# Kernel tuning notes

Measured on AMD Instinct MI355X. Metric: run time of the kernel, lower is better.

The kernel has to match this reference:

```python
import jax, jax.numpy as jnp
import numpy as np
from jax import lax

B, S, I, H, O = 64, 512, 512, 1024, 2


def setup_inputs() -> dict:
    key = jax.random.key(0)
    ks = jax.random.split(key, 16)
    sc = 0.02
    def w(k, shape):
        return jax.random.normal(k, shape, dtype=jnp.float32) * sc
    inp = {
        "x": jax.random.normal(ks[0], (B, S, I), dtype=jnp.float32),
        # layer 0 GRU gates: Linear(I+H, H)
        "Wr0": w(ks[1], (H, I + H)), "br0": jnp.zeros((H,), jnp.float32),
        "Wz0": w(ks[2], (H, I + H)), "bz0": jnp.zeros((H,), jnp.float32),
        "Wc0": w(ks[3], (H, I + H)), "bc0": jnp.zeros((H,), jnp.float32),
        # layer 1 GRU gates: Linear(H+H, H)
        "Wr1": w(ks[4], (H, 2 * H)), "br1": jnp.zeros((H,), jnp.float32),
        "Wz1": w(ks[5], (H, 2 * H)), "bz1": jnp.zeros((H,), jnp.float32),
        "Wc1": w(ks[6], (H, 2 * H)), "bc1": jnp.zeros((H,), jnp.float32),
        "Wreg": w(ks[7], (O, H)), "breg": jnp.zeros((O,), jnp.float32),
    }
    return inp


def _gru_cell(h, xin, Wr, br, Wz, bz, Wc, bc):
    # Faithful to source GRUCell: note h*z + (1-z)*can (inverted vs standard GRU).
    xh = jnp.concatenate([xin, h], axis=1)
    r = jax.nn.sigmoid(xh @ Wr.T + br)
    z = jax.nn.sigmoid(xh @ Wz.T + bz)
    can = jnp.tanh(jnp.concatenate([xin, h * r], axis=1) @ Wc.T + bc)
    return h * z + (1.0 - z) * can


def reference(x, Wr0, br0, Wz0, bz0, Wc0, bc0, Wr1, br1, Wz1, bz1, Wc1, bc1, Wreg, breg):
    b = x.shape[0]
    hdim = Wr0.shape[0]
    h0_init = jnp.zeros((b, hdim), x.dtype)
    h1_init = jnp.zeros((b, hdim), x.dtype)

    def step(carry, xt):
        h0, h1 = carry
        h0 = _gru_cell(h0, xt, Wr0, br0, Wz0, bz0, Wc0, bc0)
        h1 = _gru_cell(h1, h0, Wr1, br1, Wz1, bz1, Wc1, bc1)
        return (h0, h1), None

    xs = jnp.swapaxes(x, 0, 1)  # [S, B, I]
    (h0, h1), _ = lax.scan(step, (h0_init, h1_init), xs)
    return h1 @ Wreg.T + breg
```

## Files before the change

### kernel.cpp

```cpp
#include <hip/hip_runtime.h>


typedef _Float16 f16;
typedef f16  f16x8 __attribute__((ext_vector_type(8)));
typedef float f32x4 __attribute__((ext_vector_type(4)));
typedef unsigned long long u64;

#define NB   64
#define SEQ  512
#define IDIM 512
#define HDIM 1024
#define NBH  (NB*HDIM)

#define OFF_H0   0u
#define OFF_H1   262144u
#define OFF_H0R  524288u
#define OFF_H1R  655360u
#define OFF_FLA  786432u
#define OFF_FLB  787456u
#define OFF_W16  790528u
#define W16_L0_ELEMS 4718592u

#define SMEM_BYTES 37888

#define MFMA16 __builtin_amdgcn_mfma_f32_16x16x32_f16

__device__ __forceinline__ float sigf(float x){ return 1.0f/(1.0f+__expf(-x)); }
__device__ __forceinline__ float tanh_fast(float x){ float e=__expf(2.0f*x); return 1.0f - 2.0f/(e+1.0f); }

__device__ __forceinline__ f16x8 cload16(const f16* p){
  f16x8 r;
  asm volatile("global_load_dwordx4 %0, %1, off sc0 sc1" : "=v"(r) : "v"(p));
  return r;
}
__device__ __forceinline__ void cstore16(f16* p, f16x8 v){
  asm volatile("global_store_dwordx4 %0, %1, off sc0 sc1" :: "v"(p), "v"(v) : "memory");
}

__device__ __forceinline__ f16x8 load_x_frag(const float* p){
  f32x4 v0 = *(const f32x4*)p;
  f32x4 v1 = *(const f32x4*)(p+4);
  f16x8 r;
  r[0]=(f16)v0[0]; r[1]=(f16)v0[1]; r[2]=(f16)v0[2]; r[3]=(f16)v0[3];
  r[4]=(f16)v1[0]; r[5]=(f16)v1[1]; r[6]=(f16)v1[2]; r[7]=(f16)v1[3];
  return r;
}

template<int LAYER>
__device__ void run_rnn(int g, int n32, const float* x,
    const float* brp, const float* bzp, const float* bcp,
    char* ws, char* smem, unsigned* flA, unsigned* flB, int slotB){
  constexpr int K   = (LAYER==0) ? 1536 : 2048;
  constexpr int NKS = K/32;
  constexpr int KW  = NKS/8;
  constexpr int XKS = (LAYER==0) ? 16 : 32;
  const int tid  = threadIdx.x;
  const int lane = tid & 63;
  const int kg   = tid >> 6;
  const int quad = lane >> 4;
  const int qo   = quad*8;
  const int m_base = g*16;
  const int n_base = n32*32;
  const int arow   = m_base + (lane & 15);

  f32x4* red = (f32x4*)smem;
  float* zst = (float*)(smem + 32768);
  f16*   hst = (f16*)  (smem + 34816);
  float* hf  = (float*)(smem + 35840);

  hf[tid & 511] = 0.f;
  __syncthreads();

  f16* h0m = (f16*)(ws + OFF_H0);
  f16* h1m = (f16*)(ws + OFF_H1);
  f16* hrbuf = (LAYER==0) ? (f16*)(ws + OFF_H0R) : (f16*)(ws + OFF_H1R);
  f16* hown  = (LAYER==0) ? h0m : h1m;
  const char* w16L = ws + OFF_W16 + (LAYER ? (size_t)W16_L0_ELEMS*2 : 0);

  const size_t lo = (size_t)lane*16;
  const int nt0 = n32*2, nt1 = n32*2 + 1;
  const char* bR0 = w16L + ((size_t)((0*64 + nt0)*NKS + kg*KW))*1024 + lo;
  const char* bR1 = w16L + ((size_t)((0*64 + nt1)*NKS + kg*KW))*1024 + lo;
  const char* bZ0 = w16L + ((size_t)((1*64 + nt0)*NKS + kg*KW))*1024 + lo;
  const char* bZ1 = w16L + ((size_t)((1*64 + nt1)*NKS + kg*KW))*1024 + lo;
  const char* bC0 = w16L + ((size_t)((2*64 + nt0)*NKS + kg*KW))*1024 + lo;
  const char* bC1 = w16L + ((size_t)((2*64 + nt1)*NKS + kg*KW))*1024 + lo;

  const int col_own = n_base + (kg & 1)*16 + (lane & 15);
  const float bRv = brp[col_own], bZv = bzp[col_own], bCv = bcp[col_own];

  unsigned lgA = 0, lgB = 0;
  f16x8 fa[KW];
  f16x8 xf[KW];

  if (LAYER==0){
#pragma unroll
    for (int j=0;j<KW;++j){
      int ks = kg*KW + j;
      if (ks < XKS) xf[j] = load_x_frag(x + ((size_t)arow*SEQ + 0)*IDIM + ks*32 + qo);
    }
  }

  for (int iter = 0; iter <= SEQ; ++iter){
    const bool act  = (LAYER==0) ? (iter < SEQ) : (iter >= 1);
    const int  bufA = (iter & 1) ^ 1;

    f32x4 aC0{0,0,0,0}, aC1{0,0,0,0};

    if (act){
#pragma unroll
      for (int j=0;j<KW;++j){
        int ks = kg*KW + j;
        if (LAYER==0){
          if (ks >= XKS)
            fa[j] = cload16(h0m + (size_t)bufA*NBH + (size_t)arow*HDIM + (ks-16)*32 + qo);
        } else {
          if (ks < 32)
            fa[j] = cload16(h0m + (size_t)bufA*NBH + (size_t)arow*HDIM + ks*32 + qo);
          else
            fa[j] = cload16(h1m + (size_t)(iter&1)*NBH + (size_t)arow*HDIM + (ks-32)*32 + qo);
        }
      }
      f16x8 wA[KW], wB[KW];
#pragma unroll
      for (int j=0;j<KW;++j){
        wA[j] = *(const f16x8*)(bR0 + j*1024);
        wB[j] = *(const f16x8*)(bR1 + j*1024);
      }
      asm volatile("s_waitcnt vmcnt(0)" ::: "memory");
      __builtin_amdgcn_sched_barrier(0);
      f32x4 aR0{0,0,0,0}, aR1{0,0,0,0};
#pragma unroll
      for (int j=0;j<KW;++j){
        int ks = kg*KW + j;
        const f16x8 a = (LAYER==0 && ks < XKS) ? xf[j] : fa[j];
        aR0 = MFMA16(a, wA[j], aR0, 0,0,0);
        aR1 = MFMA16(a, wB[j], aR1, 0,0,0);
      }
      red[(0*8+kg)*64+lane] = aR0;
      red[(1*8+kg)*64+lane] = aR1;
    }
    __syncthreads();
    if (act && kg < 2){
      f32x4 s = red[(kg*8+0)*64+lane];
#pragma unroll
      for (int k2=1;k2<8;++k2) s += red[(kg*8+k2)*64+lane];
      const int coll = kg*16 + (lane & 15);
#pragma unroll
      for (int i=0;i<4;++i){
        int rowl = quad*4 + i;
        float r = sigf(s[i] + bRv);
        hst[rowl*32 + coll] = (f16)(hf[rowl*32 + coll] * r);
      }
    }
    __syncthreads();
    if (act && tid < 64){
      int rowl = tid >> 2, c8 = (tid & 3)*8;
      f16x8 v = *(const f16x8*)(hst + rowl*32 + c8);
      cstore16(hrbuf + (size_t)(m_base+rowl)*HDIM + n_base + c8, v);
    }
    asm volatile("s_waitcnt vmcnt(0) lgkmcnt(0)" ::: "memory");
    ++lgA;
    if (tid == 0)
      __hip_atomic_store(flA + n32, lgA, __ATOMIC_RELAXED, __HIP_MEMORY_SCOPE_AGENT);

    if (act){
      f16x8 wA[KW], wB[KW];
#pragma unroll
      for (int j=0;j<KW;++j){
        wA[j] = *(const f16x8*)(bZ0 + j*1024);
        wB[j] = *(const f16x8*)(bZ1 + j*1024);
      }
      f32x4 aZ0{0,0,0,0}, aZ1{0,0,0,0};
#pragma unroll
      for (int j=0;j<KW;++j){
        int ks = kg*KW + j;
        const f16x8 a = (LAYER==0 && ks < XKS) ? xf[j] : fa[j];
        aZ0 = MFMA16(a, wA[j], aZ0, 0,0,0);
        aZ1 = MFMA16(a, wB[j], aZ1, 0,0,0);
      }
      red[(2*8+kg)*64+lane] = aZ0;
      red[(3*8+kg)*64+lane] = aZ1;
#pragma unroll
      for (int j=0;j<KW;++j){
        int ks = kg*KW + j;
        if (ks < XKS){
          const f16x8 a = (LAYER==0) ? xf[j] : fa[j];
          aC0 = MFMA16(a, *(const f16x8*)(bC0 + j*1024), aC0, 0,0,0);
          aC1 = MFMA16(a, *(const f16x8*)(bC1 + j*1024), aC1, 0,0,0);
        }
      }
    }
    __syncthreads();
    if (act && (kg == 2 || kg == 3)){
      f32x4 s = red[(kg*8+0)*64+lane];
#pragma unroll
      for (int k2=1;k2<8;++k2) s += red[(kg*8+k2)*64+lane];
      const int coll = (kg & 1)*16 + (lane & 15);
#pragma unroll
      for (int i=0;i<4;++i)
        zst[(quad*4+i)*32 + coll] = sigf(s[i] + bZv);
    }
    if (tid < 32){
      while (__hip_atomic_load(flA + tid, __ATOMIC_RELAXED, __HIP_MEMORY_SCOPE_AGENT) < lgA) {}
    }
    __syncthreads();

    if (act && (kg+1)*KW > XKS){
#pragma unroll
      for (int j=0;j<KW;++j){
        int ks = kg*KW + j;
        if (ks >= XKS)
          fa[j] = cload16(hrbuf + (size_t)arow*HDIM + (ks-XKS)*32 + qo);
      }
      f16x8 wA[KW], wB[KW];
#pragma unroll
      for (int j=0;j<KW;++j){
        int ks = kg*KW + j;
        if (ks >= XKS){
          wA[j] = *(const f16x8*)(bC0 + j*1024);
          wB[j] = *(const f16x8*)(bC1 + j*1024);
        }
      }
      asm volatile("s_waitcnt vmcnt(0)" ::: "memory");
      __builtin_amdgcn_sched_barrier(0);
#pragma unroll
      for (int j=0;j<KW;++j){
        int ks = kg*KW + j;
        if (ks >= XKS){
          aC0 = MFMA16(fa[j], wA[j], aC0, 0,0,0);
          aC1 = MFMA16(fa[j], wB[j], aC1, 0,0,0);
        }
      }
    }
    if (act){
      red[(0*8+kg)*64+lane] = aC0;
      red[(1*8+kg)*64+lane] = aC1;
    }
    __syncthreads();
    if (act && kg < 2){
      f32x4 s = red[(kg*8+0)*64+lane];
#pragma unroll
      for (int k2=1;k2<8;++k2) s += red[(kg*8+k2)*64+lane];
      const int coll = kg*16 + (lane & 15);
#pragma unroll
      for (int i=0;i<4;++i){
        int rowl = quad*4 + i;
        float can = tanh_fast(s[i] + bCv);
        float z   = zst[rowl*32 + coll];
        float hnew = hf[rowl*32 + coll]*z + (1.0f - z)*can;
        hf[rowl*32 + coll]  = hnew;
        hst[rowl*32 + coll] = (f16)hnew;
      }
    }
    __syncthreads();
    if (act && tid < 64){
      const int bufW = (LAYER==0) ? (iter&1) : ((iter&1)^1);
      int rowl = tid >> 2, c8 = (tid & 3)*8;
      f16x8 v = *(const f16x8*)(hst + rowl*32 + c8);
      cstore16(hown + (size_t)bufW*NBH + (size_t)(m_base+rowl)*HDIM + n_base + c8, v);
    }
    asm volatile("s_waitcnt vmcnt(0) lgkmcnt(0)" ::: "memory");
    ++lgB;
    if (tid == 0)
      __hip_atomic_store(flB + slotB, lgB, __ATOMIC_RELAXED, __HIP_MEMORY_SCOPE_AGENT);
    if (LAYER==0 && iter+1 < SEQ){
#pragma unroll
      for (int j=0;j<KW;++j){
        int ks = kg*KW + j;
        if (ks < XKS)
          xf[j] = load_x_frag(x + ((size_t)arow*SEQ + (iter+1))*IDIM + ks*32 + qo);
      }
    }
    if (tid < 64){
      while (__hip_atomic_load(flB + tid, __ATOMIC_RELAXED, __HIP_MEMORY_SCOPE_AGENT) < lgB) {}
    }
    __syncthreads();
  }
}

__global__ void __launch_bounds__(512, 2)
rnn_kernel(const float* x,
           const float* br0, const float* bz0, const float* bc0,
           const float* br1, const float* bz1, const float* bc1,
           const float* Wreg, const float* breg,
           float* out, char* ws){
  extern __shared__ char smem[];
  const int b = blockIdx.x;
  const int xcd = b & 7, slot = b >> 3;
  const int g = slot & 3, phi = slot >> 2;
  const int p = phi*8 + xcd;
  const int layer = p >> 5, n32 = p & 31;
  unsigned* flA = (unsigned*)(ws + OFF_FLA) + (g*2 + layer)*32;
  unsigned* flB = (unsigned*)(ws + OFF_FLB) + g*64;
  const int slotB = layer*32 + n32;

  if (layer==0) run_rnn<0>(g, n32, x, br0,bz0,bc0, ws, smem, flA, flB, slotB);
  else          run_rnn<1>(g, n32, x, br1,bz1,bc1, ws, smem, flA, flB, slotB);

  if (layer==1 && n32==0 && threadIdx.x < 32){
    int mrow = g*16 + ((int)threadIdx.x >> 1), o = threadIdx.x & 1;
    const _Float16* hp = (const _Float16*)(ws + OFF_H1) + (size_t)NBH + (size_t)mrow*HDIM;
    const float* wp = Wreg + (size_t)o*HDIM;
    float acc = 0.f;
#pragma unroll 4
    for (int k=0;k<HDIM;k+=4){
      u64 q = __hip_atomic_load((const u64*)(hp+k), __ATOMIC_RELAXED, __HIP_MEMORY_SCOPE_AGENT);
      union { u64 qq; _Float16 h[4]; } u; u.qq = q;
      acc += (float)u.h[0]*wp[k]   + (float)u.h[1]*wp[k+1]
           + (float)u.h[2]*wp[k+2] + (float)u.h[3]*wp[k+3];
    }
    out[mrow*2 + o] = acc + breg[o];
  }
}

__global__ void prep_w(const float* Wr0, const float* Wz0, const float* Wc0,
                       const float* Wr1, const float* Wz1, const float* Wc1,
                       f16* w16){
  size_t i = (size_t)blockIdx.x*256 + threadIdx.x;
  const bool l1 = (i >= (size_t)W16_L0_ELEMS);
  size_t j = l1 ? i - (size_t)W16_L0_ELEMS : i;
  const int K   = l1 ? 2048 : 1536;
  const int NKS = K >> 5;
  int e    = (int)(j & 7);
  int lane = (int)((j >> 3) & 63);
  size_t r = j >> 9;
  int ks   = (int)(r % (size_t)NKS);
  size_t gnt = r / (size_t)NKS;
  int nt   = (int)(gnt & 63);
  int gate = (int)(gnt >> 6);
  int n = nt*16 + (lane & 15);
  int k = ks*32 + ((lane >> 4) << 3) + e;
  const float* W = l1 ? (gate==0 ? Wr1 : gate==1 ? Wz1 : Wc1)
                      : (gate==0 ? Wr0 : gate==1 ? Wz0 : Wc0);
  w16[i] = (f16)W[(size_t)n*K + k];
}

extern "C" void kernel_launch(void* const* d_in, const int* in_sizes, int n_in,
                              void* d_out, int out_size, void* d_ws, size_t ws_size,
                              hipStream_t stream){
  const float* x    = (const float*)d_in[0];
  const float* Wr0  = (const float*)d_in[1];
  const float* br0  = (const float*)d_in[2];
  const float* Wz0  = (const float*)d_in[3];
  const float* bz0  = (const float*)d_in[4];
  const float* Wc0  = (const float*)d_in[5];
  const float* bc0  = (const float*)d_in[6];
  const float* Wr1  = (const float*)d_in[7];
  const float* br1  = (const float*)d_in[8];
  const float* Wz1  = (const float*)d_in[9];
  const float* bz1  = (const float*)d_in[10];
  const float* Wc1  = (const float*)d_in[11];
  const float* bc1  = (const float*)d_in[12];
  const float* Wreg = (const float*)d_in[13];
  const float* breg = (const float*)d_in[14];
  float* out = (float*)d_out;
  char*  ws  = (char*)d_ws;

  hipMemsetAsync(ws, 0, OFF_W16, stream);

  prep_w<<<43008, 256, 0, stream>>>(Wr0, Wz0, Wc0, Wr1, Wz1, Wc1,
                                    (f16*)(ws + OFF_W16));

  hipFuncSetAttribute((const void*)rnn_kernel,
                      hipFuncAttributeMaxDynamicSharedMemorySize, 160*1024);

  void* args[] = { (void*)&x,
                   (void*)&br0, (void*)&bz0, (void*)&bc0,
                   (void*)&br1, (void*)&bz1, (void*)&bc1,
                   (void*)&Wreg, (void*)&breg,
                   (void*)&out, (void*)&ws };
  hipLaunchCooperativeKernel((const void*)rnn_kernel, dim3(256), dim3(512),
                             args, (unsigned)SMEM_BYTES, stream);
}
```

Baseline: 5.757 ms.

## Replace block-wide flag barriers with per-wave targeted polling on needed producers

Removes the end-of-iteration global barrier and the mid-step flA barrier. Each wave now polls only the flags of the producer blocks whose hidden-state slices it actually reads, using wave-wide __all with s_sleep. Weight loads are issued before polling so they overlap the wait. Layer 0 also waits on the other layer's flags before overwriting its h buffer, to avoid a write-after-read race, and the regressor waits for the final flags. This loosens cross-block synchronisation so steps can overlap, at the cost of subtler correctness around buffer reuse.

```diff
diff --git a/kernel.cpp b/kernel.cpp
--- a/kernel.cpp
+++ b/kernel.cpp
@@ -46,10 +46,24 @@
   return r;
 }
 
+__device__ __forceinline__ void poll_flags(const unsigned* f, int base, int cnt,
+                                           unsigned tgt){
+  if (cnt <= 0) return;
+  const int lane = (int)(threadIdx.x & 63);
+  const unsigned* p = f + base + (lane < cnt ? lane : 0);
+  for (;;){
+    unsigned v = __hip_atomic_load(p, __ATOMIC_RELAXED, __HIP_MEMORY_SCOPE_AGENT);
+    bool ok = (lane >= cnt) || (v >= tgt);
+    if (__all(ok)) return;
+    __builtin_amdgcn_s_sleep(1);
+  }
+}
+
 template<int LAYER>
 __device__ void run_rnn(int g, int n32, const float* x,
     const float* brp, const float* bzp, const float* bcp,
-    char* ws, char* smem, unsigned* flA, unsigned* flB, int slotB){
+    char* ws, char* smem,
+    unsigned* flA, const unsigned* flAo, unsigned* flB, int slotB){
   constexpr int K   = (LAYER==0) ? 1536 : 2048;
   constexpr int NKS = K/32;
   constexpr int KW  = NKS/8;
@@ -89,6 +103,13 @@
   const int col_own = n_base + (kg & 1)*16 + (lane & 15);
   const float bRv = brp[col_own], bZv = bzp[col_own], bCv = bcp[col_own];
 
+  const int aLo   = (kg*KW < (LAYER==0?16:0)) ? (LAYER==0?16:0) : kg*KW;
+  const int aBase = (LAYER==0) ? (aLo - 16) : aLo;
+  const int aCnt  = kg*KW + KW - aLo;
+  const int bLo   = (kg*KW < XKS) ? XKS : kg*KW;
+  const int bBase = bLo - XKS;
+  const int bCnt  = kg*KW + KW - bLo;
+
   unsigned lgA = 0, lgB = 0;
   f16x8 fa[KW];
   f16x8 xf[KW];
@@ -108,6 +129,13 @@
     f32x4 aC0{0,0,0,0}, aC1{0,0,0,0};
 
     if (act){
+      f16x8 wA[KW], wB[KW];
+#pragma unroll
+      for (int j=0;j<KW;++j){
+        wA[j] = *(const f16x8*)(bR0 + j*1024);
+        wB[j] = *(const f16x8*)(bR1 + j*1024);
+      }
+      poll_flags(flB, aBase, aCnt, lgB);
 #pragma unroll
       for (int j=0;j<KW;++j){
         int ks = kg*KW + j;
@@ -121,12 +149,6 @@
             fa[j] = cload16(h1m + (size_t)(iter&1)*NBH + (size_t)arow*HDIM + (ks-32)*32 + qo);
         }
       }
-      f16x8 wA[KW], wB[KW];
-#pragma unroll
-      for (int j=0;j<KW;++j){
-        wA[j] = *(const f16x8*)(bR0 + j*1024);
-        wB[j] = *(const f16x8*)(bR1 + j*1024);
-      }
       asm volatile("s_waitcnt vmcnt(0)" ::: "memory");
       __builtin_amdgcn_sched_barrier(0);
       f32x4 aR0{0,0,0,0}, aR1{0,0,0,0};
@@ -201,18 +223,8 @@
       for (int i=0;i<4;++i)
         zst[(quad*4+i)*32 + coll] = sigf(s[i] + bZv);
     }
-    if (tid < 32){
-      while (__hip_atomic_load(flA + tid, __ATOMIC_RELAXED, __HIP_MEMORY_SCOPE_AGENT) < lgA) {}
-    }
-    __syncthreads();
-
-    if (act && (kg+1)*KW > XKS){
-#pragma unroll
-      for (int j=0;j<KW;++j){
-        int ks = kg*KW + j;
-        if (ks >= XKS)
-          fa[j] = cload16(hrbuf + (size_t)arow*HDIM + (ks-XKS)*32 + qo);
-      }
+
+    if (act && bCnt > 0){
       f16x8 wA[KW], wB[KW];
 #pragma unroll
       for (int j=0;j<KW;++j){
@@ -221,6 +233,13 @@
           wA[j] = *(const f16x8*)(bC0 + j*1024);
           wB[j] = *(const f16x8*)(bC1 + j*1024);
         }
+      }
+      poll_flags(flA, bBase, bCnt, lgA);
+#pragma unroll
+      for (int j=0;j<KW;++j){
+        int ks = kg*KW + j;
+        if (ks >= XKS)
+          fa[j] = cload16(hrbuf + (size_t)arow*HDIM + (ks-XKS)*32 + qo);
       }
       asm volatile("s_waitcnt vmcnt(0)" ::: "memory");
       __builtin_amdgcn_sched_barrier(0);
@@ -255,6 +274,7 @@
     }
     __syncthreads();
     if (act && tid < 64){
+      if (LAYER==0) poll_flags(flAo, 0, 32, lgA - 1);
       const int bufW = (LAYER==0) ? (iter&1) : ((iter&1)^1);
       int rowl = tid >> 2, c8 = (tid & 3)*8;
       f16x8 v = *(const f16x8*)(hst + rowl*32 + c8);
@@ -272,10 +292,6 @@
           xf[j] = load_x_frag(x + ((size_t)arow*SEQ + (iter+1))*IDIM + ks*32 + qo);
       }
     }
-    if (tid < 64){
-      while (__hip_atomic_load(flB + tid, __ATOMIC_RELAXED, __HIP_MEMORY_SCOPE_AGENT) < lgB) {}
-    }
-    __syncthreads();
   }
 }
 
@@ -291,14 +307,16 @@
   const int g = slot & 3, phi = slot >> 2;
   const int p = phi*8 + xcd;
   const int layer = p >> 5, n32 = p & 31;
-  unsigned* flA = (unsigned*)(ws + OFF_FLA) + (g*2 + layer)*32;
-  unsigned* flB = (unsigned*)(ws + OFF_FLB) + g*64;
+  unsigned* flA  = (unsigned*)(ws + OFF_FLA) + (g*2 + layer)*32;
+  unsigned* flAo = (unsigned*)(ws + OFF_FLA) + (g*2 + (layer^1))*32;
+  unsigned* flB  = (unsigned*)(ws + OFF_FLB) + g*64;
   const int slotB = layer*32 + n32;
 
-  if (layer==0) run_rnn<0>(g, n32, x, br0,bz0,bc0, ws, smem, flA, flB, slotB);
-  else          run_rnn<1>(g, n32, x, br1,bz1,bc1, ws, smem, flA, flB, slotB);
+  if (layer==0) run_rnn<0>(g, n32, x, br0,bz0,bc0, ws, smem, flA, flAo, flB, slotB);
+  else          run_rnn<1>(g, n32, x, br1,bz1,bc1, ws, smem, flA, flAo, flB, slotB);
 
   if (layer==1 && n32==0 && threadIdx.x < 32){
+    poll_flags(flB, 32, 32, SEQ + 1);
     int mrow = g*16 + ((int)threadIdx.x >> 1), o = threadIdx.x & 1;
     const _Float16* hp = (const _Float16*)(ws + OFF_H1) + (size_t)NBH + (size_t)mrow*HDIM;
     const float* wp = Wreg + (size_t)o*HDIM;
```

Result: slower. 7.101 ms (+23.4%).
